# Optimization experiments

Hardware: AMD Instinct MI355X
Metric: run time of the kernel (lower is better)

## Reference

```python
import jax, jax.numpy as jnp
import numpy as np

ALPHA = 0.3


def _maxsim_scores(q, d):
    # q: [B, N, D], d: [C, S, D] -> scores [B, C]
    # MaxSim: per (query b, doc c), sum over query tokens of max over doc tokens.
    sim = jnp.einsum('bnd,csd->bcns', q, d)  # [B, C, N, S]
    return sim.max(axis=3).sum(axis=2)       # [B, C]


def setup_inputs() -> dict:
    key = jax.random.key(0)
    k1, k2, k3, k4 = jax.random.split(key, 4)
    B, N, S, D = 64, 32, 1024, 128
    return {
        'query_embeddings': jax.random.normal(k1, (B, N, D), dtype=jnp.float32),
        'doc_embeddings': jax.random.normal(k2, (B, S, D), dtype=jnp.float32),
        'teacher_query_outputs': jax.random.normal(k3, (B, N, D), dtype=jnp.float32),
        'teacher_doc_outputs': jax.random.normal(k4, (B, S, D), dtype=jnp.float32),
    }


def reference(query_embeddings, doc_embeddings, teacher_query_outputs, teacher_doc_outputs):
    scores = _maxsim_scores(query_embeddings, doc_embeddings)  # [B, B]
    B = scores.shape[0]
    pos_scores = jnp.diag(scores)                               # [B]
    eye = jnp.eye(B, dtype=bool)
    s_masked = jnp.where(eye, -jnp.inf, scores)
    neg_scores = s_masked.max(axis=1)                           # hardest negative per query
    contrastive_loss = jax.nn.softplus(neg_scores - pos_scores).mean()

    teacher_scores = _maxsim_scores(teacher_query_outputs, teacher_doc_outputs)
    # Torch MSELoss on fp16-cast inputs: compute in fp16, then promote.
    diff16 = scores.astype(jnp.float16) - teacher_scores.astype(jnp.float16)
    mse_loss = jnp.mean(diff16 * diff16).astype(jnp.float32)

    return contrastive_loss + ALPHA * mse_loss
```

## Files before the change

### kernel.cpp

```cpp
#include <hip/hip_runtime.h>
#include <hip/hip_bf16.h>

typedef __attribute__((ext_vector_type(8))) short short8;
typedef __attribute__((ext_vector_type(4))) float floatx4;

#define B_SZ   64
#define N_TOK  32
#define S_TOK  1024
#define D_DIM  128
#define ALPHA  0.3f

#define STRIP_S     64
#define STRIP_BYTES (STRIP_S * D_DIM * 4)
#define NSTRIP      (S_TOK / STRIP_S)
#define C_EL        (S_TOK * D_DIM)
#define QN          ((size_t)B_SZ * N_TOK * D_DIM)

__device__ __forceinline__ short f2bf(float f) {
    __hip_bfloat16 h = __float2bfloat16(f);
    return __builtin_bit_cast(short, h);
}

__device__ __forceinline__ short8 cvt8(const float* __restrict__ p) {
    floatx4 f0 = *reinterpret_cast<const floatx4*>(p);
    floatx4 f1 = *reinterpret_cast<const floatx4*>(p + 4);
    short8 r;
    r[0] = f2bf(f0[0]); r[1] = f2bf(f0[1]); r[2] = f2bf(f0[2]); r[3] = f2bf(f0[3]);
    r[4] = f2bf(f1[0]); r[5] = f2bf(f1[1]); r[6] = f2bf(f1[2]); r[7] = f2bf(f1[3]);
    return r;
}

__global__ __launch_bounds__(256) void cvt_q_kernel(
    const float* __restrict__ q, const float* __restrict__ tq,
    __hip_bfloat16* __restrict__ qb, __hip_bfloat16* __restrict__ tqb) {
    const float* src = blockIdx.y ? tq : q;
    __hip_bfloat16* dst = blockIdx.y ? tqb : qb;
    int idx = blockIdx.x * 256 + threadIdx.x;
    *reinterpret_cast<short8*>(dst + (size_t)idx * 8) = cvt8(src + (size_t)idx * 8);
}

__device__ __forceinline__ void gload_lds16(const void* g, void* l) {
    __builtin_amdgcn_global_load_lds(
        (const __attribute__((address_space(1))) unsigned int*)g,
        (__attribute__((address_space(3))) unsigned int*)l, 16, 0, 0);
}

__global__ __launch_bounds__(256, 2) void maxsim_scores_kernel(
    const __hip_bfloat16* __restrict__ qb, const __hip_bfloat16* __restrict__ tqb,
    const float* __restrict__ d, const float* __restrict__ td,
    float* __restrict__ scores_ws ) {

    const int c     = blockIdx.x;
    const int bg    = blockIdx.y;
    const int which = blockIdx.z;
    const __hip_bfloat16* Q = which ? tqb : qb;
    const float*          D = which ? td  : d;
    float* out = scores_ws + which * (B_SZ * B_SZ);

    const int tid = threadIdx.x;
    const int w   = tid >> 6;
    const int l   = tid & 63;
    const int lg  = l >> 4;
    const int lr  = l & 15;

    const int b0 = bg * 16 + w * 4;

    __shared__ __align__(16) char smem[2 * STRIP_BYTES];

    short8 afrag[8][4];
#pragma unroll
    for (int mt = 0; mt < 8; ++mt)
#pragma unroll
        for (int ks = 0; ks < 4; ++ks)
            afrag[mt][ks] = *reinterpret_cast<const short8*>(
                Q + ((size_t)(b0 + (mt >> 1)) * N_TOK + (mt & 1) * 16 + lr) * D_DIM
                  + ks * 32 + lg * 8);
#pragma unroll
    for (int mt = 0; mt < 8; ++mt)
#pragma unroll
        for (int ks = 0; ks < 4; ++ks)
            asm volatile("" : "+v"(afrag[mt][ks]));

    float runmax[8][4];
#pragma unroll
    for (int mt = 0; mt < 8; ++mt)
#pragma unroll
        for (int j = 0; j < 4; ++j) runmax[mt][j] = -INFINITY;

    const floatx4 fzero = {0.f, 0.f, 0.f, 0.f};

    unsigned goff[8];
#pragma unroll
    for (int i = 0; i < 8; ++i) {
        int g   = i * 256 + tid;
        int sub = g >> 10;
        int chq = (g >> 7) & 7;
        int eh  = (g >> 6) & 1;
        int li  = g & 63;
        int ks  = chq >> 1, nt = chq & 1;
        int lg2 = li >> 4,  lr2 = li & 15;
        int s_local = sub * 32 + nt * 16 + lr2;
        int k       = ks * 32 + lg2 * 8 + eh * 4;
        goff[i] = (unsigned)((s_local * D_DIM + k) * 4);
    }

    const char* gstrip = (const char*)(D + (size_t)c * C_EL);

#pragma unroll
    for (int i = 0; i < 8; ++i)
        gload_lds16(gstrip + goff[i], smem + i * 4096 + tid * 16);
    __syncthreads();

    for (int st = 0; st < NSTRIP; ++st) {
        const char* bufc = smem + (size_t)(st & 1) * STRIP_BYTES;

        if (st + 1 < NSTRIP) {
            const char* gs = gstrip + (size_t)(st + 1) * STRIP_BYTES;
            char* bufn = smem + (size_t)((st + 1) & 1) * STRIP_BYTES;
#pragma unroll
            for (int i = 0; i < 8; ++i)
                gload_lds16(gs + goff[i], bufn + i * 4096 + tid * 16);
        }

#pragma unroll
        for (int ph = 0; ph < 4; ++ph) {
            const char* base = bufc + (ph >> 1) * 16384 + (ph & 1) * 2048;

            short8 bf[4];
#pragma unroll
            for (int ks = 0; ks < 4; ++ks) {
                floatx4 lo = *reinterpret_cast<const floatx4*>(base + ks * 4096 + l * 16);
                floatx4 hi = *reinterpret_cast<const floatx4*>(base + ks * 4096 + 1024 + l * 16);
                short8 r;
                r[0] = f2bf(lo[0]); r[1] = f2bf(lo[1]); r[2] = f2bf(lo[2]); r[3] = f2bf(lo[3]);
                r[4] = f2bf(hi[0]); r[5] = f2bf(hi[1]); r[6] = f2bf(hi[2]); r[7] = f2bf(hi[3]);
                bf[ks] = r;
            }

            floatx4 acc[8];
#pragma unroll
            for (int mt = 0; mt < 8; ++mt)
                acc[mt] = __builtin_amdgcn_mfma_f32_16x16x32_bf16(
                    afrag[mt][0], bf[0], fzero, 0, 0, 0);
#pragma unroll
            for (int ks = 1; ks < 4; ++ks)
#pragma unroll
                for (int mt = 0; mt < 8; ++mt)
                    acc[mt] = __builtin_amdgcn_mfma_f32_16x16x32_bf16(
                        afrag[mt][ks], bf[ks], acc[mt], 0, 0, 0);

#pragma unroll
            for (int mt = 0; mt < 8; ++mt)
#pragma unroll
                for (int j = 0; j < 4; ++j)
                    runmax[mt][j] = fmaxf(runmax[mt][j], acc[mt][j]);
        }

        __syncthreads();
    }

#pragma unroll
    for (int mt = 0; mt < 8; ++mt)
#pragma unroll
        for (int j = 0; j < 4; ++j) {
            float v = runmax[mt][j];
            v = fmaxf(v, __shfl_xor(v, 1));
            v = fmaxf(v, __shfl_xor(v, 2));
            v = fmaxf(v, __shfl_xor(v, 4));
            v = fmaxf(v, __shfl_xor(v, 8));
            runmax[mt][j] = v;
        }

#pragma unroll
    for (int p = 0; p < 4; ++p) {
        float s = 0.f;
#pragma unroll
        for (int j = 0; j < 4; ++j) s += runmax[2 * p][j] + runmax[2 * p + 1][j];
        s += __shfl_xor(s, 16);
        s += __shfl_xor(s, 32);
        if (l == 0) out[(b0 + p) * B_SZ + c] = s;
    }
}

__global__ void loss_kernel(const float* __restrict__ scores_ws, float* __restrict__ out) {
    const float* sc = scores_ws;
    const float* tc = scores_ws + B_SZ * B_SZ;
    const int b = threadIdx.x;

    float pos = sc[b * B_SZ + b];
    float neg = -INFINITY;
    float msesum = 0.f;
#pragma unroll 8
    for (int cc = 0; cc < B_SZ; ++cc) {
        float s = sc[b * B_SZ + cc];
        float t = tc[b * B_SZ + cc];
        if (cc != b) neg = fmaxf(neg, s);
        _Float16 d16 = (_Float16)s - (_Float16)t;
        _Float16 sq  = d16 * d16;
        msesum += (float)sq;
    }
    float x = neg - pos;
    float sp = (x > 0.f) ? (x + log1pf(expf(-x))) : log1pf(expf(x));

#pragma unroll
    for (int m = 1; m < 64; m <<= 1) {
        sp     += __shfl_xor(sp, m);
        msesum += __shfl_xor(msesum, m);
    }
    if (b == 0) {
        float mse = msesum / 4096.f;
        mse = (float)(_Float16)mse;
        out[0] = sp / 64.f + ALPHA * mse;
    }
}

extern "C" void kernel_launch(void* const* d_in, const int* in_sizes, int n_in,
                              void* d_out, int out_size, void* d_ws, size_t ws_size,
                              hipStream_t stream) {
    const float* q  = (const float*)d_in[0];
    const float* d  = (const float*)d_in[1];
    const float* tq = (const float*)d_in[2];
    const float* td = (const float*)d_in[3];
    float* out = (float*)d_out;

    float* scores_ws = (float*)d_ws;
    __hip_bfloat16* qb  = (__hip_bfloat16*)((char*)d_ws + 32768);
    __hip_bfloat16* tqb = qb + QN;

    cvt_q_kernel<<<dim3((unsigned)(QN / 8 / 256), 2), 256, 0, stream>>>(q, tq, qb, tqb);

    dim3 grid(B_SZ, B_SZ / 16, 2);
    maxsim_scores_kernel<<<grid, 256, 0, stream>>>(qb, tqb, d, td, scores_ws);
    loss_kernel<<<1, 64, 0, stream>>>(scores_ws, out);
}
```

Baseline: 89.15 us.

## Fuse query bf16 conversion into maxsim kernel and use swizzled row-major doc strips

Drops the separate query fp32-to-bf16 conversion kernel; each block now loads fp32 query fragments and converts them in registers, which saves a launch and a workspace round trip. Doc strips shrink from 64 to 32 tokens and are staged into LDS in contiguous row-major order with an XOR swizzle, replacing the fragment-permuted gather addresses. This is meant to keep global loads contiguous while avoiding LDS bank conflicts. In exchange, the duplicated query conversion costs more global reads per block, and the smaller strips mean twice as many barrier iterations.

```diff
diff --git a/kernel.cpp b/kernel.cpp
--- a/kernel.cpp
+++ b/kernel.cpp
@@ -10,33 +10,14 @@
 #define D_DIM  128
 #define ALPHA  0.3f
 
-#define STRIP_S     64
+#define STRIP_S     32
 #define STRIP_BYTES (STRIP_S * D_DIM * 4)
 #define NSTRIP      (S_TOK / STRIP_S)
 #define C_EL        (S_TOK * D_DIM)
-#define QN          ((size_t)B_SZ * N_TOK * D_DIM)
 
 __device__ __forceinline__ short f2bf(float f) {
     __hip_bfloat16 h = __float2bfloat16(f);
     return __builtin_bit_cast(short, h);
-}
-
-__device__ __forceinline__ short8 cvt8(const float* __restrict__ p) {
-    floatx4 f0 = *reinterpret_cast<const floatx4*>(p);
-    floatx4 f1 = *reinterpret_cast<const floatx4*>(p + 4);
-    short8 r;
-    r[0] = f2bf(f0[0]); r[1] = f2bf(f0[1]); r[2] = f2bf(f0[2]); r[3] = f2bf(f0[3]);
-    r[4] = f2bf(f1[0]); r[5] = f2bf(f1[1]); r[6] = f2bf(f1[2]); r[7] = f2bf(f1[3]);
-    return r;
-}
-
-__global__ __launch_bounds__(256) void cvt_q_kernel(
-    const float* __restrict__ q, const float* __restrict__ tq,
-    __hip_bfloat16* __restrict__ qb, __hip_bfloat16* __restrict__ tqb) {
-    const float* src = blockIdx.y ? tq : q;
-    __hip_bfloat16* dst = blockIdx.y ? tqb : qb;
-    int idx = blockIdx.x * 256 + threadIdx.x;
-    *reinterpret_cast<short8*>(dst + (size_t)idx * 8) = cvt8(src + (size_t)idx * 8);
 }
 
 __device__ __forceinline__ void gload_lds16(const void* g, void* l) {
@@ -45,16 +26,20 @@
         (__attribute__((address_space(3))) unsigned int*)l, 16, 0, 0);
 }
 
+__device__ __forceinline__ unsigned swz(unsigned y) {
+    return y ^ (((y >> 9) & 7) << 4);
+}
+
 __global__ __launch_bounds__(256, 2) void maxsim_scores_kernel(
-    const __hip_bfloat16* __restrict__ qb, const __hip_bfloat16* __restrict__ tqb,
-    const float* __restrict__ d, const float* __restrict__ td,
+    const float* __restrict__ qf, const float* __restrict__ tqf,
+    const float* __restrict__ d,  const float* __restrict__ td,
     float* __restrict__ scores_ws ) {
 
     const int c     = blockIdx.x;
     const int bg    = blockIdx.y;
     const int which = blockIdx.z;
-    const __hip_bfloat16* Q = which ? tqb : qb;
-    const float*          D = which ? td  : d;
+    const float* Q = which ? tqf : qf;
+    const float* D = which ? td  : d;
     float* out = scores_ws + which * (B_SZ * B_SZ);
 
     const int tid = threadIdx.x;
@@ -71,10 +56,16 @@
 #pragma unroll
     for (int mt = 0; mt < 8; ++mt)
 #pragma unroll
-        for (int ks = 0; ks < 4; ++ks)
-            afrag[mt][ks] = *reinterpret_cast<const short8*>(
-                Q + ((size_t)(b0 + (mt >> 1)) * N_TOK + (mt & 1) * 16 + lr) * D_DIM
-                  + ks * 32 + lg * 8);
+        for (int ks = 0; ks < 4; ++ks) {
+            const float* qp = Q + ((size_t)(b0 + (mt >> 1)) * N_TOK + (mt & 1) * 16 + lr) * D_DIM
+                                + ks * 32 + lg * 8;
+            floatx4 f0 = *reinterpret_cast<const floatx4*>(qp);
+            floatx4 f1 = *reinterpret_cast<const floatx4*>(qp + 4);
+            short8 r;
+            r[0] = f2bf(f0[0]); r[1] = f2bf(f0[1]); r[2] = f2bf(f0[2]); r[3] = f2bf(f0[3]);
+            r[4] = f2bf(f1[0]); r[5] = f2bf(f1[1]); r[6] = f2bf(f1[2]); r[7] = f2bf(f1[3]);
+            afrag[mt][ks] = r;
+        }
 #pragma unroll
     for (int mt = 0; mt < 8; ++mt)
 #pragma unroll
@@ -89,27 +80,21 @@
 
     const floatx4 fzero = {0.f, 0.f, 0.f, 0.f};
 
-    unsigned goff[8];
-#pragma unroll
-    for (int i = 0; i < 8; ++i) {
-        int g   = i * 256 + tid;
-        int sub = g >> 10;
-        int chq = (g >> 7) & 7;
-        int eh  = (g >> 6) & 1;
-        int li  = g & 63;
-        int ks  = chq >> 1, nt = chq & 1;
-        int lg2 = li >> 4,  lr2 = li & 15;
-        int s_local = sub * 32 + nt * 16 + lr2;
-        int k       = ks * 32 + lg2 * 8 + eh * 4;
-        goff[i] = (unsigned)((s_local * D_DIM + k) * 4);
-    }
-
     const char* gstrip = (const char*)(D + (size_t)c * C_EL);
 
-#pragma unroll
-    for (int i = 0; i < 8; ++i)
-        gload_lds16(gstrip + goff[i], smem + i * 4096 + tid * 16);
+    unsigned ydst[4], ysrc[4];
+#pragma unroll
+    for (int i = 0; i < 4; ++i) {
+        ydst[i] = i * 4096 + tid * 16;
+        ysrc[i] = swz(ydst[i]);
+    }
+
+#pragma unroll
+    for (int i = 0; i < 4; ++i)
+        gload_lds16(gstrip + ysrc[i], smem + ydst[i]);
     __syncthreads();
+
+    const unsigned xr = ((unsigned)(lr & 7)) << 4;
 
     for (int st = 0; st < NSTRIP; ++st) {
         const char* bufc = smem + (size_t)(st & 1) * STRIP_BYTES;
@@ -118,22 +103,23 @@
             const char* gs = gstrip + (size_t)(st + 1) * STRIP_BYTES;
             char* bufn = smem + (size_t)((st + 1) & 1) * STRIP_BYTES;
 #pragma unroll
-            for (int i = 0; i < 8; ++i)
-                gload_lds16(gs + goff[i], bufn + i * 4096 + tid * 16);
-        }
-
-#pragma unroll
-        for (int ph = 0; ph < 4; ++ph) {
-            const char* base = bufc + (ph >> 1) * 16384 + (ph & 1) * 2048;
+            for (int i = 0; i < 4; ++i)
+                gload_lds16(gs + ysrc[i], bufn + ydst[i]);
+        }
+
+#pragma unroll
+        for (int nt = 0; nt < 2; ++nt) {
+            const unsigned rowbyte = (unsigned)((nt * 16 + lr) * 512);
 
             short8 bf[4];
 #pragma unroll
             for (int ks = 0; ks < 4; ++ks) {
-                floatx4 lo = *reinterpret_cast<const floatx4*>(base + ks * 4096 + l * 16);
-                floatx4 hi = *reinterpret_cast<const floatx4*>(base + ks * 4096 + 1024 + l * 16);
+                unsigned lo = (rowbyte + (unsigned)(ks * 128 + lg * 32)) ^ xr;
+                floatx4 f0 = *reinterpret_cast<const floatx4*>(bufc + lo);
+                floatx4 f1 = *reinterpret_cast<const floatx4*>(bufc + (lo ^ 16u));
                 short8 r;
-                r[0] = f2bf(lo[0]); r[1] = f2bf(lo[1]); r[2] = f2bf(lo[2]); r[3] = f2bf(lo[3]);
-                r[4] = f2bf(hi[0]); r[5] = f2bf(hi[1]); r[6] = f2bf(hi[2]); r[7] = f2bf(hi[3]);
+                r[0] = f2bf(f0[0]); r[1] = f2bf(f0[1]); r[2] = f2bf(f0[2]); r[3] = f2bf(f0[3]);
+                r[4] = f2bf(f1[0]); r[5] = f2bf(f1[1]); r[6] = f2bf(f1[2]); r[7] = f2bf(f1[3]);
                 bf[ks] = r;
             }
 
@@ -224,12 +210,8 @@
     float* out = (float*)d_out;
 
     float* scores_ws = (float*)d_ws;
-    __hip_bfloat16* qb  = (__hip_bfloat16*)((char*)d_ws + 32768);
-    __hip_bfloat16* tqb = qb + QN;
-
-    cvt_q_kernel<<<dim3((unsigned)(QN / 8 / 256), 2), 256, 0, stream>>>(q, tq, qb, tqb);
 
     dim3 grid(B_SZ, B_SZ / 16, 2);
-    maxsim_scores_kernel<<<grid, 256, 0, stream>>>(qb, tqb, d, td, scores_ws);
+    maxsim_scores_kernel<<<grid, 256, 0, stream>>>(q, tq, d, td, scores_ws);
     loss_kernel<<<1, 64, 0, stream>>>(scores_ws, out);
 }
```

Result: faster. 80.61 us (-9.6%).
